# Kernel tuning notes

Measured on AMD Instinct MI355X. Metric: run time of the kernel, lower is better.

The kernel has to match this reference:

```python
import jax, jax.numpy as jnp
import numpy as np

B, N, F_IN, F_OUT = 8, 2048, 64, 64
ALPHA = 0.2  # LeakyReLU negative slope


def setup_inputs() -> dict:
    key = jax.random.key(0)
    k_in, k_adj, k_w, k_a1, k_a2 = jax.random.split(key, 5)
    inp = jax.random.normal(k_in, (B, N, F_IN), dtype=jnp.float32)
    adj = (jax.random.uniform(k_adj, (B, N, N)) < 0.05).astype(jnp.float32)
    # xavier_uniform with gain=sqrt(2)
    def xavier(k, shape):
        fan_in, fan_out = shape[0], shape[1]
        bound = np.sqrt(2.0) * np.sqrt(6.0 / (fan_in + fan_out))
        return jax.random.uniform(k, shape, jnp.float32, -bound, bound)
    W = xavier(k_w, (F_IN, F_OUT))
    a1 = xavier(k_a1, (F_OUT, 1))
    a2 = xavier(k_a2, (F_OUT, 1))
    bias = jnp.full((N, F_OUT), 0.1, dtype=jnp.float32)
    return {"input": inp, "adj": adj, "W": W, "a1": a1, "a2": a2, "bias": bias}


def reference(input, adj, W, a1, a2, bias):
    # h: [B, N, F_OUT]
    h = jnp.einsum("bnf,fo->bno", input, W)
    f1 = h @ a1          # [B, N, 1]
    f2 = h @ a2          # [B, N, 1]
    e = jax.nn.leaky_relu(f1 + jnp.swapaxes(f2, 1, 2), negative_slope=ALPHA)  # [B, N, N]
    # NOTE: original multiplies adj elementwise (not -inf mask) and softmaxes over dim=1
    attention = jax.nn.softmax(adj * e, axis=1)
    h_prime = jnp.einsum("bij,bjo->bio", attention, h) + bias  # bias broadcasts over batch
    h_prime = h_prime + input  # in_features == out_features, no downsample
    return jax.nn.elu(h_prime)
```

## Files before the change

kernel.cpp:

```cpp
#include <hip/hip_runtime.h>
#include <cstdint>
#include <cstddef>

#define Bn 8
#define Nn 2048
#define Fn 64
#define ALPHA 0.2f
#define CAPR 192

typedef __attribute__((ext_vector_type(4))) float f4vec;

__device__ __forceinline__ float elu(float x) { return x > 0.f ? x : __expf(x) - 1.f; }
__device__ __forceinline__ float4 ntload4(const float* p) {
    f4vec v = __builtin_nontemporal_load((const f4vec*)p);
    return make_float4(v.x, v.y, v.z, v.w);
}

__global__ __launch_bounds__(256) void k1_h_f(
        const float* __restrict__ inp, const float* __restrict__ W,
        const float* __restrict__ a1, const float* __restrict__ a2,
        float* __restrict__ h, float* __restrict__ f1, float* __restrict__ f2,
        float* __restrict__ Dsum, float* __restrict__ C) {
    __shared__ float Wl[Fn * Fn];
    __shared__ float inr[4 * Fn];
    int t = threadIdx.x;
    if (blockIdx.x < 64) Dsum[blockIdx.x * 256 + t] = 0.f;
    else if (blockIdx.x == 64) { C[t] = 0.f; C[t + 256] = 0.f; }
    for (int k = t; k < Fn * Fn; k += 256) Wl[k] = W[k];
    size_t row0 = (size_t)blockIdx.x * 4;
    inr[t] = inp[row0 * Fn + t];
    __syncthreads();
    int r = t >> 6, o = t & 63;
    const float* irow = &inr[r * Fn];
    float acc = 0.f;
#pragma unroll
    for (int f = 0; f < Fn; ++f) acc = fmaf(irow[f], Wl[f * Fn + o], acc);
    size_t row = row0 + r;
    h[row * Fn + o] = acc;
    float p = acc * a1[o];
    float q = acc * a2[o];
#pragma unroll
    for (int off = 32; off > 0; off >>= 1) {
        p += __shfl_down(p, off, 64);
        q += __shfl_down(q, off, 64);
    }
    if (o == 0) { f1[row] = p; f2[row] = q; }
}

__global__ __launch_bounds__(512) void k2a_bits(
        const float* __restrict__ adj, const float* __restrict__ f1,
        const float* __restrict__ f2,
        float* __restrict__ Dsum, unsigned* __restrict__ bitsW) {
    int b = blockIdx.x;
    int j0 = blockIdx.y * 256;
    int cj8 = blockIdx.y * 8;
    int i0 = blockIdx.z * 64;
    int w = threadIdx.x >> 6, lane = threadIdx.x & 63;
    float4 f2v = *(const float4*)&f2[b * Nn + j0 + 4 * lane];
    float vh0 = __expf(f2v.x), vp0 = __expf(ALPHA * f2v.x);
    float vh1 = __expf(f2v.y), vp1 = __expf(ALPHA * f2v.y);
    float vh2 = __expf(f2v.z), vp2 = __expf(ALPHA * f2v.z);
    float vh3 = __expf(f2v.w), vp3 = __expf(ALPHA * f2v.w);
    float s0 = 0.f, s1 = 0.f, s2 = 0.f, s3 = 0.f;
    const float* abase = adj + ((size_t)b * Nn) * Nn + j0 + 4 * lane;
    const float* f1b = f1 + b * Nn;

    float4 av[8]; float fi[8];
#pragma unroll
    for (int q = 0; q < 8; ++q) {
        int r = i0 + w + 8 * q;
        av[q] = ntload4(abase + (size_t)r * Nn);
        fi[q] = f1b[r];
    }
#pragma unroll
    for (int q = 0; q < 8; ++q) {
        int r = i0 + w + 8 * q;
        float u  = __expf(fi[q]);
        float up = __expf(ALPHA * fi[q]);
        bool n0 = av[q].x != 0.f, n1 = av[q].y != 0.f,
             n2 = av[q].z != 0.f, n3 = av[q].w != 0.f;
        float x0 = fi[q] + f2v.x, x1 = fi[q] + f2v.y,
              x2 = fi[q] + f2v.z, x3 = fi[q] + f2v.w;
        float e0 = x0 > 0.f ? u * vh0 : up * vp0;
        float e1 = x1 > 0.f ? u * vh1 : up * vp1;
        float e2 = x2 > 0.f ? u * vh2 : up * vp2;
        float e3 = x3 > 0.f ? u * vh3 : up * vp3;
        s0 += n0 ? e0 : 1.0f;
        s1 += n1 ? e1 : 1.0f;
        s2 += n2 ? e2 : 1.0f;
        s3 += n3 ? e3 : 1.0f;
        unsigned nib = (unsigned)n0 | ((unsigned)n1 << 1) |
                       ((unsigned)n2 << 2) | ((unsigned)n3 << 3);
        unsigned byt = nib | (((unsigned)__shfl_xor((int)nib, 1, 64)) << 4);
        unsigned h16 = byt | (((unsigned)__shfl_xor((int)byt, 2, 64)) << 8);
        unsigned w32 = h16 | (((unsigned)__shfl_xor((int)h16, 4, 64)) << 16);
        if ((lane & 7) == 0)
            bitsW[(size_t)(b * Nn + r) * 64 + cj8 + (lane >> 3)] = w32;
    }
    __shared__ float sred[8][256];
    sred[w][4 * lane + 0] = s0;
    sred[w][4 * lane + 1] = s1;
    sred[w][4 * lane + 2] = s2;
    sred[w][4 * lane + 3] = s3;
    __syncthreads();
    if (threadIdx.x < 256) {
        int c = threadIdx.x;
        float v = 0.f;
#pragma unroll
        for (int k = 0; k < 8; ++k) v += sred[k][c];
        atomicAdd(&Dsum[b * Nn + j0 + c], v);
    }
}

__global__ __launch_bounds__(256) void k2b_cols(
        const float* __restrict__ h, const float* __restrict__ Dsum,
        const float* __restrict__ f2,
        float4* __restrict__ cf4, float* __restrict__ C) {
    int b = blockIdx.x;
    int j0 = blockIdx.y * 64;
    int t = threadIdx.x;
    __shared__ float zl[64];
    if (t < 64) {
        int j = j0 + t;
        float f2j = f2[b * Nn + j];
        float invD = 1.f / Dsum[b * Nn + j];
        cf4[b * Nn + j] = make_float4(f2j, __expf(f2j) * invD,
                                      __expf(ALPHA * f2j) * invD, invD);
        zl[t] = invD;
    }
    __syncthreads();
    int o = t & 63, g = t >> 6;
    const float* hbp = h + ((size_t)(b * Nn + j0 + g * 16)) * Fn + o;
    float s = 0.f;
#pragma unroll
    for (int k = 0; k < 16; ++k) s = fmaf(zl[g * 16 + k], hbp[(size_t)k * Fn], s);
    atomicAdd(&C[b * Fn + o], s);
}

__global__ __launch_bounds__(256) void k3_row(
        const unsigned* __restrict__ bits, const float4* __restrict__ cf4,
        const float* __restrict__ f1, const float* __restrict__ h,
        const float* __restrict__ C, const float* __restrict__ inp,
        const float* __restrict__ bias, float* __restrict__ out) {
    int w = threadIdx.x >> 6, lane = threadIdx.x & 63;
    int b = blockIdx.x >> 9;
    int i = ((blockIdx.x & 511) << 2) + w;
    int gr = (int)(blockIdx.x * 4) + w;
    __shared__ unsigned offs[4][CAPR];
    __shared__ float wvs[4][CAPR];

    unsigned word = bits[(size_t)gr * 64 + lane];
    unsigned pc = (unsigned)__popc(word);
    unsigned pre = pc;
#pragma unroll
    for (int off = 1; off < 64; off <<= 1) {
        unsigned v = (unsigned)__shfl_up((int)pre, off, 64);
        if (lane >= off) pre += v;
    }
    unsigned base = pre - pc;
    unsigned jb8 = ((unsigned)lane * 32u) << 8;
    while (word) {
        int k = __ffs(word) - 1;
        word &= word - 1;
        if (base < CAPR) offs[w][base] = jb8 + ((unsigned)k << 8);
        ++base;
    }
    unsigned cnt = (unsigned)__shfl((int)pre, 63, 64);
    if (cnt > CAPR) cnt = CAPR;

    float f1i = f1[gr];
    float ui = __expf(f1i), upi = __expf(ALPHA * f1i);
    const float4* cfp = cf4 + (size_t)b * Nn;

    size_t g = (size_t)gr * Fn + lane;
    float inv = inp[g];
    float bvv = bias[(size_t)i * Fn + lane];
    float Cv  = C[b * Fn + lane];

    {
        unsigned ta = lane, tb = lane + 64u, tc = lane + 128u;
        bool va = ta < cnt, vb = tb < cnt, vc = tc < cnt;
        float4 ca, cb, cc;
        if (va) ca = cfp[offs[w][ta] >> 8];
        if (vb) cb = cfp[offs[w][tb] >> 8];
        if (vc) cc = cfp[offs[w][tc] >> 8];
        if (va) { float x = f1i + ca.x; wvs[w][ta] = (x > 0.f ? ui * ca.y : upi * ca.z) - ca.w; }
        if (vb) { float x = f1i + cb.x; wvs[w][tb] = (x > 0.f ? ui * cb.y : upi * cb.z) - cb.w; }
        if (vc) { float x = f1i + cc.x; wvs[w][tc] = (x > 0.f ? ui * cc.y : upi * cc.z) - cc.w; }
    }

    const char* hbase = (const char*)(h + (size_t)b * Nn * Fn);
    unsigned lane4 = (unsigned)lane << 2;
    float acc0 = 0.f, acc1 = 0.f, acc2 = 0.f, acc3 = 0.f;
    unsigned t = 0;
    for (; t + 16 <= cnt; t += 16) {
        uint4 oa = *(const uint4*)&offs[w][t];
        uint4 ob = *(const uint4*)&offs[w][t + 4];
        uint4 oc = *(const uint4*)&offs[w][t + 8];
        uint4 od = *(const uint4*)&offs[w][t + 12];
        float4 wa = *(const float4*)&wvs[w][t];
        float4 wb = *(const float4*)&wvs[w][t + 4];
        float4 wc = *(const float4*)&wvs[w][t + 8];
        float4 wd = *(const float4*)&wvs[w][t + 12];
        float h0 = *(const float*)(hbase + (oa.x + lane4));
        float h1 = *(const float*)(hbase + (oa.y + lane4));
        float h2 = *(const float*)(hbase + (oa.z + lane4));
        float h3 = *(const float*)(hbase + (oa.w + lane4));
        float h4 = *(const float*)(hbase + (ob.x + lane4));
        float h5 = *(const float*)(hbase + (ob.y + lane4));
        float h6 = *(const float*)(hbase + (ob.z + lane4));
        float h7 = *(const float*)(hbase + (ob.w + lane4));
        float h8 = *(const float*)(hbase + (oc.x + lane4));
        float h9 = *(const float*)(hbase + (oc.y + lane4));
        float hA = *(const float*)(hbase + (oc.z + lane4));
        float hB = *(const float*)(hbase + (oc.w + lane4));
        float hC = *(const float*)(hbase + (od.x + lane4));
        float hD = *(const float*)(hbase + (od.y + lane4));
        float hE = *(const float*)(hbase + (od.z + lane4));
        float hF = *(const float*)(hbase + (od.w + lane4));
        acc0 = fmaf(wa.x, h0, acc0);
        acc1 = fmaf(wa.y, h1, acc1);
        acc2 = fmaf(wa.z, h2, acc2);
        acc3 = fmaf(wa.w, h3, acc3);
        acc0 = fmaf(wb.x, h4, acc0);
        acc1 = fmaf(wb.y, h5, acc1);
        acc2 = fmaf(wb.z, h6, acc2);
        acc3 = fmaf(wb.w, h7, acc3);
        acc0 = fmaf(wc.x, h8, acc0);
        acc1 = fmaf(wc.y, h9, acc1);
        acc2 = fmaf(wc.z, hA, acc2);
        acc3 = fmaf(wc.w, hB, acc3);
        acc0 = fmaf(wd.x, hC, acc0);
        acc1 = fmaf(wd.y, hD, acc1);
        acc2 = fmaf(wd.z, hE, acc2);
        acc3 = fmaf(wd.w, hF, acc3);
    }
    for (; t + 4 <= cnt; t += 4) {
        uint4 oa = *(const uint4*)&offs[w][t];
        float4 wa = *(const float4*)&wvs[w][t];
        float h0 = *(const float*)(hbase + (oa.x + lane4));
        float h1 = *(const float*)(hbase + (oa.y + lane4));
        float h2 = *(const float*)(hbase + (oa.z + lane4));
        float h3 = *(const float*)(hbase + (oa.w + lane4));
        acc0 = fmaf(wa.x, h0, acc0);
        acc1 = fmaf(wa.y, h1, acc1);
        acc2 = fmaf(wa.z, h2, acc2);
        acc3 = fmaf(wa.w, h3, acc3);
    }
    for (; t < cnt; ++t) {
        float hv = *(const float*)(hbase + (offs[w][t] + lane4));
        acc0 = fmaf(wvs[w][t], hv, acc0);
    }
    float v = (acc0 + acc1) + (acc2 + acc3) + Cv;
    out[g] = elu(v + inv + bvv);
}

extern "C" void kernel_launch(void* const* d_in, const int* in_sizes, int n_in,
                              void* d_out, int out_size, void* d_ws, size_t ws_size,
                              hipStream_t stream) {
    const float* inp  = (const float*)d_in[0];
    const float* adj  = (const float*)d_in[1];
    const float* W    = (const float*)d_in[2];
    const float* a1   = (const float*)d_in[3];
    const float* a2   = (const float*)d_in[4];
    const float* bias = (const float*)d_in[5];
    float* out = (float*)d_out;

    char* ws = (char*)d_ws;
    unsigned* bitsW = (unsigned*)ws;
    float*  h     = (float*)(ws + 4194304);
    float4* cf4   = (float4*)(ws + 8388608);
    float*  f1    = (float*)(ws + 8650752);
    float*  f2    = (float*)(ws + 8716288);
    float*  Dsum  = (float*)(ws + 8781824);
    float*  C     = (float*)(ws + 8847360);

    k1_h_f<<<Bn * Nn / 4, 256, 0, stream>>>(inp, W, a1, a2, h, f1, f2, Dsum, C);
    k2a_bits<<<dim3(Bn, 8, 32), 512, 0, stream>>>(adj, f1, f2, Dsum, bitsW);
    k2b_cols<<<dim3(Bn, Nn / 64), 256, 0, stream>>>(h, Dsum, f2, cf4, C);
    k3_row<<<Bn * Nn / 4, 256, 0, stream>>>(bitsW, cf4, f1, h, C, inp, bias, out);
}
```

Baseline: 238.6 us.

## Fuse column-normalization kernel into bitmask kernel via last-block atomic counter

Removes the separate k2b_cols launch. Each column strip of k2a_bits now increments a per-(batch, strip) counter, and the last of the 32 row-blocks to finish computes the inverse column sums, writes cf4, and accumulates the C contribution from h. This saves one kernel launch and its gap, but adds a threadfence/atomic handshake, a tail of work done by only a few blocks, and more shared memory per block.

```diff
diff --git a/kernel.cpp b/kernel.cpp
--- a/kernel.cpp
+++ b/kernel.cpp
@@ -20,12 +20,15 @@
         const float* __restrict__ inp, const float* __restrict__ W,
         const float* __restrict__ a1, const float* __restrict__ a2,
         float* __restrict__ h, float* __restrict__ f1, float* __restrict__ f2,
-        float* __restrict__ Dsum, float* __restrict__ C) {
+        float* __restrict__ Dsum, float* __restrict__ C, unsigned* __restrict__ cnt) {
     __shared__ float Wl[Fn * Fn];
     __shared__ float inr[4 * Fn];
     int t = threadIdx.x;
     if (blockIdx.x < 64) Dsum[blockIdx.x * 256 + t] = 0.f;
-    else if (blockIdx.x == 64) { C[t] = 0.f; C[t + 256] = 0.f; }
+    else if (blockIdx.x == 64) {
+        C[t] = 0.f; C[t + 256] = 0.f;
+        if (t < 64) cnt[t] = 0u;
+    }
     for (int k = t; k < Fn * Fn; k += 256) Wl[k] = W[k];
     size_t row0 = (size_t)blockIdx.x * 4;
     inr[t] = inp[row0 * Fn + t];
@@ -49,11 +52,16 @@
 
 __global__ __launch_bounds__(512) void k2a_bits(
         const float* __restrict__ adj, const float* __restrict__ f1,
-        const float* __restrict__ f2,
-        float* __restrict__ Dsum, unsigned* __restrict__ bitsW) {
+        const float* __restrict__ f2, const float* __restrict__ h,
+        float* __restrict__ Dsum, unsigned* __restrict__ bitsW,
+        float4* __restrict__ cf4, float* __restrict__ C, unsigned* __restrict__ cnt) {
+    __shared__ float sred[8][256];
+    __shared__ float invDs[256];
+    __shared__ bool lastf;
     int b = blockIdx.x;
-    int j0 = blockIdx.y * 256;
-    int cj8 = blockIdx.y * 8;
+    int jy = blockIdx.y;
+    int j0 = jy * 256;
+    int cj8 = jy * 8;
     int i0 = blockIdx.z * 64;
     int w = threadIdx.x >> 6, lane = threadIdx.x & 63;
     float4 f2v = *(const float4*)&f2[b * Nn + j0 + 4 * lane];
@@ -97,7 +105,6 @@
         if ((lane & 7) == 0)
             bitsW[(size_t)(b * Nn + r) * 64 + cj8 + (lane >> 3)] = w32;
     }
-    __shared__ float sred[8][256];
     sred[w][4 * lane + 0] = s0;
     sred[w][4 * lane + 1] = s1;
     sred[w][4 * lane + 2] = s2;
@@ -110,31 +117,39 @@
         for (int k = 0; k < 8; ++k) v += sred[k][c];
         atomicAdd(&Dsum[b * Nn + j0 + c], v);
     }
-}
-
-__global__ __launch_bounds__(256) void k2b_cols(
-        const float* __restrict__ h, const float* __restrict__ Dsum,
-        const float* __restrict__ f2,
-        float4* __restrict__ cf4, float* __restrict__ C) {
-    int b = blockIdx.x;
-    int j0 = blockIdx.y * 64;
-    int t = threadIdx.x;
-    __shared__ float zl[64];
-    if (t < 64) {
-        int j = j0 + t;
-        float f2j = f2[b * Nn + j];
-        float invD = 1.f / Dsum[b * Nn + j];
-        cf4[b * Nn + j] = make_float4(f2j, __expf(f2j) * invD,
-                                      __expf(ALPHA * f2j) * invD, invD);
-        zl[t] = invD;
-    }
-    __syncthreads();
-    int o = t & 63, g = t >> 6;
-    const float* hbp = h + ((size_t)(b * Nn + j0 + g * 16)) * Fn + o;
-    float s = 0.f;
-#pragma unroll
-    for (int k = 0; k < 16; ++k) s = fmaf(zl[g * 16 + k], hbp[(size_t)k * Fn], s);
-    atomicAdd(&C[b * Fn + o], s);
+    __syncthreads();
+    if (threadIdx.x == 0) {
+        __threadfence();
+        unsigned old = atomicAdd(&cnt[b * 8 + jy], 1u);
+        lastf = (old == 31u);
+        __threadfence();
+    }
+    __syncthreads();
+    if (lastf) {
+        int t = threadIdx.x;
+        if (t < 256) {
+            int j = j0 + t;
+            float f2j = f2[b * Nn + j];
+            float invD = 1.f / Dsum[b * Nn + j];
+            cf4[b * Nn + j] = make_float4(f2j, __expf(f2j) * invD,
+                                          __expf(ALPHA * f2j) * invD, invD);
+            invDs[t] = invD;
+        }
+        __syncthreads();
+        int o = t & 63, jg = t >> 6;
+        const float* hbp = h + ((size_t)(b * Nn + j0 + jg * 32)) * Fn + o;
+        float s = 0.f;
+#pragma unroll
+        for (int k = 0; k < 32; ++k) s = fmaf(invDs[jg * 32 + k], hbp[(size_t)k * Fn], s);
+        sred[jg][o] = s;
+        __syncthreads();
+        if (t < 64) {
+            float v = 0.f;
+#pragma unroll
+            for (int k = 0; k < 8; ++k) v += sred[k][t];
+            atomicAdd(&C[b * Fn + t], v);
+        }
+    }
 }
 
 __global__ __launch_bounds__(256) void k3_row(
@@ -274,9 +289,9 @@
     float*  f2    = (float*)(ws + 8716288);
     float*  Dsum  = (float*)(ws + 8781824);
     float*  C     = (float*)(ws + 8847360);
-
-    k1_h_f<<<Bn * Nn / 4, 256, 0, stream>>>(inp, W, a1, a2, h, f1, f2, Dsum, C);
-    k2a_bits<<<dim3(Bn, 8, 32), 512, 0, stream>>>(adj, f1, f2, Dsum, bitsW);
-    k2b_cols<<<dim3(Bn, Nn / 64), 256, 0, stream>>>(h, Dsum, f2, cf4, C);
+    unsigned* cnt = (unsigned*)(ws + 8849408);
+
+    k1_h_f<<<Bn * Nn / 4, 256, 0, stream>>>(inp, W, a1, a2, h, f1, f2, Dsum, C, cnt);
+    k2a_bits<<<dim3(Bn, 8, 32), 512, 0, stream>>>(adj, f1, f2, h, Dsum, bitsW, cf4, C, cnt);
     k3_row<<<Bn * Nn / 4, 256, 0, stream>>>(bitsW, cf4, f1, h, C, inp, bias, out);
 }
```

Measured after the change: 414.5 us. 1.74x slower.
